# Kernel tuning notes

Measured on AMD Instinct MI355X. Metric: run time of the kernel, lower is better.

Reference implementation:

```python
import jax, jax.numpy as jnp
import numpy as np

N_NODES = 50000
N_EDGES = 1600000
IN_FEATS = 128
H_FEATS = 128


def setup_inputs() -> dict:
    key = jax.random.key(0)
    ks = jax.random.split(key, 10)
    feat = jax.random.normal(ks[0], (N_NODES, IN_FEATS), dtype=jnp.float32)
    src = jax.random.randint(ks[1], (N_EDGES,), 0, N_NODES, dtype=jnp.int32)
    dst = jax.random.randint(ks[2], (N_EDGES,), 0, N_NODES, dtype=jnp.int32)
    s1 = 1.0 / np.sqrt(IN_FEATS)
    s2 = 1.0 / np.sqrt(H_FEATS)
    W_self1 = jax.random.uniform(ks[3], (IN_FEATS, H_FEATS), jnp.float32, -s1, s1)
    W_neigh1 = jax.random.uniform(ks[4], (IN_FEATS, H_FEATS), jnp.float32, -s1, s1)
    b1 = jnp.zeros((H_FEATS,), jnp.float32)
    W_self2 = jax.random.uniform(ks[5], (H_FEATS, H_FEATS), jnp.float32, -s2, s2)
    W_neigh2 = jax.random.uniform(ks[6], (H_FEATS, H_FEATS), jnp.float32, -s2, s2)
    b2 = jnp.zeros((H_FEATS,), jnp.float32)
    W_fc = jax.random.uniform(ks[7], (H_FEATS, IN_FEATS), jnp.float32, -s2, s2)
    b_fc = jax.random.uniform(ks[8], (IN_FEATS,), jnp.float32, -s2, s2)
    return {
        "feat": feat, "src": src, "dst": dst,
        "W_self1": W_self1, "W_neigh1": W_neigh1, "b1": b1,
        "W_self2": W_self2, "W_neigh2": W_neigh2, "b2": b2,
        "W_fc": W_fc, "b_fc": b_fc,
    }


def _mean_agg(h, src, dst):
    # segment-mean of src features onto dst nodes; zero-in-degree -> 0 (deg clamped to 1)
    msg = jnp.take(h, src, axis=0)                      # [E, d] gather (irregular)
    summ = jax.ops.segment_sum(msg, dst, num_segments=N_NODES)  # [N, d]
    deg = jax.ops.segment_sum(jnp.ones((src.shape[0],), h.dtype), dst, num_segments=N_NODES)
    return summ / jnp.maximum(deg, 1.0)[:, None]


def _sage(h, src, dst, W_self, W_neigh, b):
    h_neigh = _mean_agg(h, src, dst)
    return h @ W_self + h_neigh @ W_neigh + b


def reference(feat, src, dst, W_self1, W_neigh1, b1, W_self2, W_neigh2, b2, W_fc, b_fc):
    h = _sage(feat, src, dst, W_self1, W_neigh1, b1)
    h = jax.nn.relu(h)
    h = _sage(h, src, dst, W_self2, W_neigh2, b2)
    return h @ W_fc + b_fc
```

## Files before the change

### kernel.cpp

```cpp
#include <hip/hip_runtime.h>
#include <hip/hip_bf16.h>

#define NN 50000
#define NE 1600000
#define F 128
#define CAP 96
#define NBUCK 391

typedef short short8 __attribute__((ext_vector_type(8)));
typedef float f32x4 __attribute__((ext_vector_type(4)));
typedef unsigned short u16x4 __attribute__((ext_vector_type(4)));
typedef unsigned short u16x8 __attribute__((ext_vector_type(8)));

__device__ inline unsigned short bf16rne(float f) {
  unsigned u = __builtin_bit_cast(unsigned, f);
  u += 0x7FFFu + ((u >> 16) & 1u);
  return (unsigned short)(u >> 16);
}
__device__ inline float bf16f(unsigned short s) {
  unsigned u = ((unsigned)s) << 16;
  return __builtin_bit_cast(float, u);
}
__device__ inline float bflo(unsigned v) { return __builtin_bit_cast(float, v << 16); }
__device__ inline float bfhi(unsigned v) { return __builtin_bit_cast(float, v & 0xFFFF0000u); }

__global__ void zero_i32(int* __restrict__ p, int n) {
  int i = blockIdx.x * blockDim.x + threadIdx.x;
  if (i < n) p[i] = 0;
}

__global__ void mat_compose(const float* __restrict__ A, const float* __restrict__ Wfc,
                            float* __restrict__ O) {
  int idx = blockIdx.x * 256 + threadIdx.x;
  int k = idx >> 7, n = idx & 127;
  float s = 0.f;
  for (int j = 0; j < 128; ++j) s += A[k * 128 + j] * Wfc[j * 128 + n];
  O[idx] = s;
}

__global__ void bias_compose(const float* __restrict__ b2, const float* __restrict__ Wfc,
                             const float* __restrict__ bfc, float* __restrict__ bout) {
  int n = threadIdx.x;
  float s = bfc[n];
  for (int k = 0; k < 128; ++k) s += b2[k] * Wfc[k * 128 + n];
  bout[n] = s;
}


__global__ __launch_bounds__(256) void ebin_hist(const int* __restrict__ dst,
                                                 int* __restrict__ ghist) {
  __shared__ int lh[512];
  int t = threadIdx.x;
  lh[t] = 0;
  lh[t + 256] = 0;
  __syncthreads();
  int base = blockIdx.x * 3125;
  for (int k = t; k < 3125; k += 256) atomicAdd(&lh[dst[base + k] >> 7], 1);
  __syncthreads();
  if (t < NBUCK && lh[t]) atomicAdd(&ghist[t], lh[t]);
  int t2 = t + 256;
  if (t2 < NBUCK && lh[t2]) atomicAdd(&ghist[t2], lh[t2]);
}

__global__ void ebin_scan(const int* __restrict__ ghist, int* __restrict__ gbase,
                          int* __restrict__ gcur) {
  __shared__ int s[512];
  int t = threadIdx.x;
  s[t] = (t < NBUCK) ? ghist[t] : 0;
  __syncthreads();
  for (int d = 1; d < 512; d <<= 1) {
    int x = (t >= d) ? s[t - d] : 0;
    __syncthreads();
    s[t] += x;
    __syncthreads();
  }
  int ex = (t == 0) ? 0 : s[t - 1];
  if (t < NBUCK) {
    gbase[t] = ex;
    gcur[t] = ex;
  }
  if (t == NBUCK) gbase[NBUCK] = s[NBUCK - 1];
}

__global__ __launch_bounds__(256) void ebin_scatter(const int* __restrict__ src,
                                                    const int* __restrict__ dst,
                                                    int* __restrict__ gcur,
                                                    unsigned* __restrict__ ebin) {
  __shared__ int lh[512], lbase[512], lcur[512];
  int t = threadIdx.x;
  lh[t] = 0; lh[t + 256] = 0;
  lcur[t] = 0; lcur[t + 256] = 0;
  __syncthreads();
  int base = blockIdx.x * 3125;
  for (int k = t; k < 3125; k += 256) atomicAdd(&lh[dst[base + k] >> 7], 1);
  __syncthreads();
  if (t < NBUCK && lh[t]) lbase[t] = atomicAdd(&gcur[t], lh[t]);
  int t2 = t + 256;
  if (t2 < NBUCK && lh[t2]) lbase[t2] = atomicAdd(&gcur[t2], lh[t2]);
  __syncthreads();
  for (int k = t; k < 3125; k += 256) {
    int d = dst[base + k];
    int b = d >> 7;
    int off = atomicAdd(&lcur[b], 1);
    ebin[lbase[b] + off] = ((unsigned)(d & 127) << 16) | (unsigned)src[base + k];
  }
}

__global__ __launch_bounds__(256) void bucket_csr(const unsigned* __restrict__ ebin,
                                                  const int* __restrict__ gbase,
                                                  int* __restrict__ cnt,
                                                  unsigned short* __restrict__ esrcPad) {
  __shared__ int lcnt[128];
  __shared__ unsigned short rows[128 * CAP];
  int t = threadIdx.x;
  int b = blockIdx.x;
  if (t < 128) lcnt[t] = 0;
  unsigned* rz = (unsigned*)rows;
  for (int i = t; i < (128 * CAP) / 2; i += 256) rz[i] = 0;
  __syncthreads();
  int s0 = gbase[b], s1 = gbase[b + 1];
  for (int i = s0 + t; i < s1; i += 256) {
    unsigned v = ebin[i];
    int dl = v >> 16;
    int p = atomicAdd(&lcnt[dl], 1);
    if (p < CAP) rows[dl * CAP + p] = (unsigned short)(v & 0xFFFFu);
  }
  __syncthreads();
  int node = b * 128 + t;
  if (t < 128 && node < NN) cnt[node] = lcnt[t];
  int nvalid = min(128, NN - b * 128);
  int limit = (nvalid * CAP) >> 1;
  const unsigned* lsrc = (const unsigned*)rows;
  unsigned* gdst = (unsigned*)(esrcPad + (size_t)b * 128 * CAP);
  for (int i = t; i < limit; i += 256) gdst[i] = lsrc[i];
}

__global__ void tobf16_chunk(const float* __restrict__ in,
                             unsigned short* __restrict__ chk,
                             unsigned short* __restrict__ X) {
  int i = blockIdx.x * 256 + threadIdx.x;
  if (i >= NN * 32) return;
  int node = i >> 5;
  int q = i & 31;
  int p = q >> 3;
  float4 v = ((const float4*)in)[i];
  u16x4 o;
  o[0] = bf16rne(v.x);
  o[1] = bf16rne(v.y);
  o[2] = bf16rne(v.z);
  o[3] = bf16rne(v.w);
  ((u16x4*)chk)[((size_t)p * NN + node) * 8 + (q & 7)] = o;
  *(u16x4*)(X + (size_t)node * 256 + q * 4) = o;
}

__global__ __launch_bounds__(256) void agg_all(const unsigned* __restrict__ tbl,
                                               const int* __restrict__ cnt,
                                               const unsigned short* __restrict__ esrcPad,
                                               unsigned short* __restrict__ X) {
  int bid = blockIdx.x;
  int xcd = bid & 7;
  int pass = xcd & 3;
  int nodeBase = (bid >> 3) * 32 + ((xcd >> 2) & 1) * 16;
  int t = threadIdx.x;
  int node = nodeBase + (t >> 4);
  if (node >= NN) return;
  const unsigned* tblp = tbl + (size_t)pass * NN * 16;
  int l = t & 15;
  int e = cnt[node];
  if (e > CAP) e = CAP;
  const unsigned short* ep = esrcPad + (size_t)node * CAP;
  float ax0 = 0.f, ay0 = 0.f, ax1 = 0.f, ay1 = 0.f;
  int nb = (e + 15) >> 4;
  for (int b = 0; b < nb; ++b) {
    int i = b * 16;
    u16x8 ua = *(const u16x8*)(ep + i);
    u16x8 ub = *(const u16x8*)(ep + i + 8);
    unsigned v[16];
#pragma unroll
    for (int j = 0; j < 8; ++j) v[j] = tblp[(size_t)ua[j] * 16 + l];
#pragma unroll
    for (int j = 0; j < 8; ++j) v[8 + j] = tblp[(size_t)ub[j] * 16 + l];
    int rem = e - i;
#pragma unroll
    for (int j = 0; j < 16; ++j) {
      unsigned x = (j < rem) ? v[j] : 0u;
      if (j & 1) { ax1 += bflo(x); ay1 += bfhi(x); }
      else       { ax0 += bflo(x); ay0 += bfhi(x); }
    }
  }
  float inv = 1.0f / (float)max(e, 1);
  unsigned w = (unsigned)bf16rne((ax0 + ax1) * inv) |
               ((unsigned)bf16rne((ay0 + ay1) * inv) << 16);
  *(unsigned*)(X + (size_t)node * 256 + 128 + pass * 32 + l * 2) = w;
}

__global__ void wprep(const float* __restrict__ Ws, const float* __restrict__ Wn,
                      unsigned short* __restrict__ hi, unsigned short* __restrict__ lo) {
  int i = blockIdx.x * 256 + threadIdx.x;
  int k = i & 255;
  int n = i >> 8;
  float w = (k < 128) ? Ws[(size_t)k * F + n] : Wn[(size_t)(k - 128) * F + n];
  unsigned short h = bf16rne(w);
  hi[i] = h;
  lo[i] = bf16rne(w - bf16f(h));
}

template <bool RELU, bool L1>
__global__ __launch_bounds__(512) void combine_mfma(
    const unsigned short* __restrict__ X,
    const unsigned short* __restrict__ WThi, const unsigned short* __restrict__ WTlo,
    const float* __restrict__ bias, float* __restrict__ Cf,
    unsigned short* __restrict__ Xout, unsigned short* __restrict__ Cb) {
  __shared__ unsigned short whs[64 * 256];
  __shared__ unsigned short wls[64 * 256];
  const int K = 256;
  int t = threadIdx.x;
  int colHalf = blockIdx.x & 1;

  {
    const unsigned short* gh = WThi + (size_t)colHalf * 64 * K;
    const unsigned short* gl = WTlo + (size_t)colHalf * 64 * K;
#pragma unroll
    for (int c = 0; c < 4; ++c) {
      int idx8 = c * 512 + t;
      int cl = idx8 >> 5;
      int byte_off = (idx8 & 31) * 16;
      int swz = byte_off ^ ((cl & 7) << 4);
      *(short8*)((char*)whs + cl * 512 + swz) = *(const short8*)(gh + (size_t)idx8 * 8);
      *(short8*)((char*)wls + cl * 512 + swz) = *(const short8*)(gl + (size_t)idx8 * 8);
    }
  }
  __syncthreads();

  int wave = t >> 6;
  int lane = t & 63;
  int lm = lane & 15;
  int lk = lane >> 4;
  int R0 = (blockIdx.x >> 1) * 128 + wave * 16;
  if (R0 < NN) {
    int rA = R0 + lm;
    if (rA >= NN) rA = NN - 1;
    short8 a[8];
    const unsigned short* xp = X + (size_t)rA * K + lk * 8;
#pragma unroll
    for (int ks = 0; ks < 8; ++ks) a[ks] = *(const short8*)(xp + ks * 32);

    f32x4 acc[4];
#pragma unroll
    for (int ct = 0; ct < 4; ++ct) {
      float b = bias[colHalf * 64 + ct * 16 + lm];
      acc[ct] = (f32x4){b, b, b, b};
    }

#pragma unroll
    for (int ct = 0; ct < 4; ++ct) {
      int cl = ct * 16 + lm;
      int cbase = cl * 512;
      int cswz = (cl & 7) << 4;
#pragma unroll
      for (int ks = 0; ks < 8; ++ks) {
        int off = cbase + ((ks * 64 + lk * 16) ^ cswz);
        short8 wh = *(const short8*)((const char*)whs + off);
        short8 wl = *(const short8*)((const char*)wls + off);
        acc[ct] = __builtin_amdgcn_mfma_f32_16x16x32_bf16(a[ks], wh, acc[ct], 0, 0, 0);
        acc[ct] = __builtin_amdgcn_mfma_f32_16x16x32_bf16(a[ks], wl, acc[ct], 0, 0, 0);
      }
    }

#pragma unroll
    for (int ct = 0; ct < 4; ++ct) {
#pragma unroll
      for (int r = 0; r < 4; ++r) {
        int row = R0 + lk * 4 + r;
        if (row < NN) {
          float v = acc[ct][r];
          if (RELU) v = fmaxf(v, 0.f);
          int col = colHalf * 64 + ct * 16 + lm;
          if (L1) {
            unsigned short b = bf16rne(v);
            Xout[(size_t)row * 256 + col] = b;
            Cb[((size_t)(col >> 5) * NN + row) * 32 + (col & 31)] = b;
          } else {
            Cf[(size_t)row * F + col] = v;
          }
        }
      }
    }
  }
}

extern "C" void kernel_launch(void* const* d_in, const int* in_sizes, int n_in,
                              void* d_out, int out_size, void* d_ws, size_t ws_size,
                              hipStream_t stream) {
  const float* feat = (const float*)d_in[0];
  const int* src = (const int*)d_in[1];
  const int* dst = (const int*)d_in[2];
  const float* Ws1 = (const float*)d_in[3];
  const float* Wn1 = (const float*)d_in[4];
  const float* b1 = (const float*)d_in[5];
  const float* Ws2 = (const float*)d_in[6];
  const float* Wn2 = (const float*)d_in[7];
  const float* b2 = (const float*)d_in[8];
  const float* Wfc = (const float*)d_in[9];
  const float* bfc = (const float*)d_in[10];
  float* out = (float*)d_out;

  unsigned short* esrcPad = (unsigned short*)d_ws;
  int* cnt = (int*)(esrcPad + (size_t)NN * CAP);
  int* ghist = cnt + 50048;
  int* gbase = ghist + 512;
  int* gcur = gbase + 512;
  unsigned* ebin = (unsigned*)(gcur + 512);
  unsigned short* X1 = (unsigned short*)(ebin + NE);
  unsigned short* X2 = X1 + (size_t)NN * 256;
  unsigned short* w1hi = X2 + (size_t)NN * 256;
  unsigned short* w1lo = w1hi + 128 * 256;
  unsigned short* w2hi = w1lo + 128 * 256;
  unsigned short* w2lo = w2hi + 128 * 256;
  float* wsf = (float*)(w2lo + 128 * 256);
  float* wnf = wsf + 128 * 128;
  float* bfF = wnf + 128 * 128;
  unsigned short* hbf = (unsigned short*)(bfF + 128);

  mat_compose<<<64, 256, 0, stream>>>(Ws2, Wfc, wsf);
  mat_compose<<<64, 256, 0, stream>>>(Wn2, Wfc, wnf);
  bias_compose<<<1, 128, 0, stream>>>(b2, Wfc, bfc, bfF);

  wprep<<<128, 256, 0, stream>>>(Ws1, Wn1, w1hi, w1lo);
  wprep<<<128, 256, 0, stream>>>(wsf, wnf, w2hi, w2lo);
  tobf16_chunk<<<(NN * 32 + 255) / 256, 256, 0, stream>>>(feat, hbf, X1);

  zero_i32<<<2, 256, 0, stream>>>(ghist, 512);
  ebin_hist<<<512, 256, 0, stream>>>(dst, ghist);
  ebin_scan<<<1, 512, 0, stream>>>(ghist, gbase, gcur);
  ebin_scatter<<<512, 256, 0, stream>>>(src, dst, gcur, ebin);
  bucket_csr<<<NBUCK, 256, 0, stream>>>(ebin, gbase, cnt, esrcPad);

  const int aggBlocks = 1563 * 8;
  const int gemBlocks = ((NN + 127) / 128) * 2;

  agg_all<<<aggBlocks, 256, 0, stream>>>((const unsigned*)hbf, cnt, esrcPad, X1);
  combine_mfma<true, true><<<gemBlocks, 512, 0, stream>>>(X1, w1hi, w1lo, b1,
                                                          nullptr, X2, hbf);

  agg_all<<<aggBlocks, 256, 0, stream>>>((const unsigned*)hbf, cnt, esrcPad, X2);
  combine_mfma<false, false><<<gemBlocks, 512, 0, stream>>>(X2, w2hi, w2lo, bfF,
                                                            out, nullptr, nullptr);
}
```

Before: 200.0 us.

## Widen gather loads to 16 bytes and pad neighbor lists with a zero row

The aggregation kernel now gives each node 4 lanes that each load a uint4 (8 bf16 values) instead of 16 lanes loading 4 bytes, so each lane issues fewer, wider gathers and keeps 8 accumulators. Empty neighbor slots now hold a sentinel index that points at an extra zeroed row in a padded feature table, so the per-element bounds select is gone and batches of 8 are summed unconditionally. This needs an NPAD stride in the table layout, a small kernel to zero the pad rows, and padded-index initialisation in the CSR build. It trades higher per-thread register use and fewer threads per node for fewer memory instructions.

```diff
diff --git a/kernel.cpp b/kernel.cpp
--- a/kernel.cpp
+++ b/kernel.cpp
@@ -2,10 +2,12 @@
 #include <hip/hip_bf16.h>
 
 #define NN 50000
+#define NPAD 50008
 #define NE 1600000
 #define F 128
 #define CAP 96
 #define NBUCK 391
+#define PADIDX 0xC350C350u
 
 typedef short short8 __attribute__((ext_vector_type(8)));
 typedef float f32x4 __attribute__((ext_vector_type(4)));
@@ -27,6 +29,14 @@
 __global__ void zero_i32(int* __restrict__ p, int n) {
   int i = blockIdx.x * blockDim.x + threadIdx.x;
   if (i < n) p[i] = 0;
+}
+
+__global__ void zero_pad(unsigned short* __restrict__ hbf) {
+  int i = threadIdx.x;
+  if (i < 512) {
+    int p = i >> 7, r = NN + ((i >> 4) & 7), d = i & 15;
+    ((unsigned*)hbf)[((size_t)p * NPAD + r) * 16 + d] = 0u;
+  }
 }
 
 __global__ void mat_compose(const float* __restrict__ A, const float* __restrict__ Wfc,
@@ -116,7 +126,7 @@
   int b = blockIdx.x;
   if (t < 128) lcnt[t] = 0;
   unsigned* rz = (unsigned*)rows;
-  for (int i = t; i < (128 * CAP) / 2; i += 256) rz[i] = 0;
+  for (int i = t; i < (128 * CAP) / 2; i += 256) rz[i] = PADIDX;
   __syncthreads();
   int s0 = gbase[b], s1 = gbase[b + 1];
   for (int i = s0 + t; i < s1; i += 256) {
@@ -149,49 +159,48 @@
   o[1] = bf16rne(v.y);
   o[2] = bf16rne(v.z);
   o[3] = bf16rne(v.w);
-  ((u16x4*)chk)[((size_t)p * NN + node) * 8 + (q & 7)] = o;
+  ((u16x4*)chk)[((size_t)p * NPAD + node) * 8 + (q & 7)] = o;
   *(u16x4*)(X + (size_t)node * 256 + q * 4) = o;
 }
 
-__global__ __launch_bounds__(256) void agg_all(const unsigned* __restrict__ tbl,
+__global__ __launch_bounds__(256) void agg_all(const uint4* __restrict__ tbl,
                                                const int* __restrict__ cnt,
                                                const unsigned short* __restrict__ esrcPad,
                                                unsigned short* __restrict__ X) {
   int bid = blockIdx.x;
   int xcd = bid & 7;
   int pass = xcd & 3;
-  int nodeBase = (bid >> 3) * 32 + ((xcd >> 2) & 1) * 16;
-  int t = threadIdx.x;
-  int node = nodeBase + (t >> 4);
+  int nodeBase = (bid >> 3) * 128 + ((xcd >> 2) & 1) * 64;
+  int t = threadIdx.x;
+  int node = nodeBase + (t >> 2);
   if (node >= NN) return;
-  const unsigned* tblp = tbl + (size_t)pass * NN * 16;
-  int l = t & 15;
+  const uint4* tblp = tbl + (size_t)pass * NPAD * 4;
+  int l = t & 3;
   int e = cnt[node];
   if (e > CAP) e = CAP;
   const unsigned short* ep = esrcPad + (size_t)node * CAP;
-  float ax0 = 0.f, ay0 = 0.f, ax1 = 0.f, ay1 = 0.f;
-  int nb = (e + 15) >> 4;
+  float acc[8];
+#pragma unroll
+  for (int j = 0; j < 8; ++j) acc[j] = 0.f;
+  int nb = (e + 7) >> 3;
   for (int b = 0; b < nb; ++b) {
-    int i = b * 16;
-    u16x8 ua = *(const u16x8*)(ep + i);
-    u16x8 ub = *(const u16x8*)(ep + i + 8);
-    unsigned v[16];
-#pragma unroll
-    for (int j = 0; j < 8; ++j) v[j] = tblp[(size_t)ua[j] * 16 + l];
-#pragma unroll
-    for (int j = 0; j < 8; ++j) v[8 + j] = tblp[(size_t)ub[j] * 16 + l];
-    int rem = e - i;
-#pragma unroll
-    for (int j = 0; j < 16; ++j) {
-      unsigned x = (j < rem) ? v[j] : 0u;
-      if (j & 1) { ax1 += bflo(x); ay1 += bfhi(x); }
-      else       { ax0 += bflo(x); ay0 += bfhi(x); }
+    u16x8 u = *(const u16x8*)(ep + b * 8);
+    uint4 v[8];
+#pragma unroll
+    for (int j = 0; j < 8; ++j) v[j] = tblp[(size_t)u[j] * 4 + l];
+#pragma unroll
+    for (int j = 0; j < 8; ++j) {
+      acc[0] += bflo(v[j].x); acc[1] += bfhi(v[j].x);
+      acc[2] += bflo(v[j].y); acc[3] += bfhi(v[j].y);
+      acc[4] += bflo(v[j].z); acc[5] += bfhi(v[j].z);
+      acc[6] += bflo(v[j].w); acc[7] += bfhi(v[j].w);
     }
   }
   float inv = 1.0f / (float)max(e, 1);
-  unsigned w = (unsigned)bf16rne((ax0 + ax1) * inv) |
-               ((unsigned)bf16rne((ay0 + ay1) * inv) << 16);
-  *(unsigned*)(X + (size_t)node * 256 + 128 + pass * 32 + l * 2) = w;
+  u16x8 o;
+#pragma unroll
+  for (int j = 0; j < 8; ++j) o[j] = bf16rne(acc[j] * inv);
+  *(u16x8*)(X + (size_t)node * 256 + 128 + pass * 32 + l * 8) = o;
 }
 
 __global__ void wprep(const float* __restrict__ Ws, const float* __restrict__ Wn,
@@ -279,7 +288,7 @@
           if (L1) {
             unsigned short b = bf16rne(v);
             Xout[(size_t)row * 256 + col] = b;
-            Cb[((size_t)(col >> 5) * NN + row) * 32 + (col & 31)] = b;
+            Cb[((size_t)(col >> 5) * NPAD + row) * 32 + (col & 31)] = b;
           } else {
             Cf[(size_t)row * F + col] = v;
           }
@@ -328,6 +337,7 @@
 
   wprep<<<128, 256, 0, stream>>>(Ws1, Wn1, w1hi, w1lo);
   wprep<<<128, 256, 0, stream>>>(wsf, wnf, w2hi, w2lo);
+  zero_pad<<<1, 512, 0, stream>>>(hbf);
   tobf16_chunk<<<(NN * 32 + 255) / 256, 256, 0, stream>>>(feat, hbf, X1);
 
   zero_i32<<<2, 256, 0, stream>>>(ghist, 512);
@@ -336,14 +346,14 @@
   ebin_scatter<<<512, 256, 0, stream>>>(src, dst, gcur, ebin);
   bucket_csr<<<NBUCK, 256, 0, stream>>>(ebin, gbase, cnt, esrcPad);
 
-  const int aggBlocks = 1563 * 8;
+  const int aggBlocks = NBUCK * 8;
   const int gemBlocks = ((NN + 127) / 128) * 2;
 
-  agg_all<<<aggBlocks, 256, 0, stream>>>((const unsigned*)hbf, cnt, esrcPad, X1);
+  agg_all<<<aggBlocks, 256, 0, stream>>>((const uint4*)hbf, cnt, esrcPad, X1);
   combine_mfma<true, true><<<gemBlocks, 512, 0, stream>>>(X1, w1hi, w1lo, b1,
                                                           nullptr, X2, hbf);
 
-  agg_all<<<aggBlocks, 256, 0, stream>>>((const unsigned*)hbf, cnt, esrcPad, X2);
+  agg_all<<<aggBlocks, 256, 0, stream>>>((const uint4*)hbf, cnt, esrcPad, X2);
   combine_mfma<false, false><<<gemBlocks, 512, 0, stream>>>(X2, w2hi, w2lo, bfF,
                                                             out, nullptr, nullptr);
 }
```

Measured after the change: 211.0 us. 5.5% more time.
